# Kernel optimization log

Measured on AMD Instinct MI355X. Metric: run time of the kernel, lower is better.

The kernel has to match this reference:

```python
import jax, jax.numpy as jnp
import numpy as np

DIM = 128
N_CODES = 1024
N_STAGES = 4
BATCH, SEQ = 16, 8192


def setup_inputs() -> dict:
    key = jax.random.key(0)
    k1, k2 = jax.random.split(key)
    x_real = jax.random.normal(k1, (BATCH, SEQ, DIM), dtype=jnp.float32)
    codebooks = jax.random.normal(k2, (N_STAGES, N_CODES, DIM), dtype=jnp.float32) * 0.02
    return {"x_real": x_real, "codebooks": codebooks}


def reference(x_real, codebooks):
    """Residual VQ: per stage compute L2 dists via matmul+norms, argmin, gather.
    Returns (quantized [B,S,dim], indices [n_stages,B,S] int32)."""
    Bshape = x_real.shape
    x_flat = x_real.reshape(-1, Bshape[-1])  # [N, dim]
    residual = x_flat
    quantized = jnp.zeros_like(x_flat)
    all_indices = []
    n_stages = codebooks.shape[0]
    for s in range(n_stages):  # small fixed stage count
        codes = codebooks[s]  # [n_codes, dim]
        dots = residual @ codes.T  # [N, n_codes]
        codes_norm = jnp.sum(codes ** 2, axis=1)[None, :]
        residual_norm = jnp.sum(residual ** 2, axis=1, keepdims=True)
        dists = residual_norm + codes_norm - 2.0 * dots
        indices = jnp.argmin(dists, axis=1)  # [N]
        chosen = codes[indices]  # [N, dim] gather
        quantized = quantized + chosen
        residual = residual - chosen
        all_indices.append(indices.reshape(Bshape[:-1]))
    q = quantized.reshape(Bshape)
    return q, jnp.stack(all_indices, axis=0)
```

## Files before the change

### kernel.cpp

```cpp
#include <hip/hip_runtime.h>
#include <hip/hip_bf16.h>
#include <math.h>

constexpr int DIM = 128;
constexpr int NC = 1024;
constexpr int NS = 4;
constexpr int NVEC = 16 * 8192;
constexpr size_t QSIZE = (size_t)NVEC * DIM;
constexpr int BM = 64;
constexpr int CAP = 32;
constexpr float MARGIN = 0.125f;
constexpr int RS = DIM + 1;
constexpr int GSZ = 8 * 64 * 8;

typedef short bf16x8 __attribute__((ext_vector_type(8)));
typedef float f32x16 __attribute__((ext_vector_type(16)));

__device__ __forceinline__ short f2bf(float f) {
    __hip_bfloat16 h = __float2bfloat16(f);
    union { __hip_bfloat16 h; short s; } u;
    u.h = h;
    return u.s;
}

__device__ __forceinline__ short f2bf_fast(float f) {
    unsigned u = __float_as_uint(f);
    unsigned r = (u + 0x7FFFu + ((u >> 16) & 1u)) >> 16;
    return (short)r;
}

__device__ __forceinline__ unsigned fmap(float f) {
    unsigned u = __float_as_uint(f);
    return (u & 0x80000000u) ? ~u : (u | 0x80000000u);
}
__device__ __forceinline__ float funmap(unsigned k) {
    unsigned u = (k & 0x80000000u) ? (k & 0x7FFFFFFFu) : ~k;
    return __uint_as_float(u);
}

template <typename PTR>
__device__ __forceinline__ float np_pairwise_sq128(PTR v) {
#pragma clang fp contract(off)
    float r[8];
#pragma unroll
    for (int j = 0; j < 8; ++j) { float sq = v[j] * v[j]; r[j] = sq; }
#pragma unroll
    for (int i = 8; i < DIM; i += 8) {
#pragma unroll
        for (int j = 0; j < 8; ++j) { float sq = v[i + j] * v[i + j]; r[j] = r[j] + sq; }
    }
    return ((r[0] + r[1]) + (r[2] + r[3])) + ((r[4] + r[5]) + (r[6] + r[7]));
}

__device__ __forceinline__ float exact_dist(const float* __restrict__ rv,
                                            const float* __restrict__ cp,
                                            float rn, float cn) {
    float a0 = 0.f;
#pragma unroll
    for (int d = 0; d < DIM; d += 4) {
        float4 q = *(const float4*)(cp + d);
        a0 = __builtin_fmaf(rv[d], q.x, a0);
        a0 = __builtin_fmaf(rv[d + 1], q.y, a0);
        a0 = __builtin_fmaf(rv[d + 2], q.z, a0);
        a0 = __builtin_fmaf(rv[d + 3], q.w, a0);
    }
    return (rn + cn) - 2.0f * a0;
}

__global__ __launch_bounds__(256) void rvq_norms(
        const float* __restrict__ cb, float* __restrict__ cnorm) {
    int row = blockIdx.x * 256 + threadIdx.x;
    if (row >= NS * NC) return;
    cnorm[row] = np_pairwise_sq128(cb + (size_t)row * DIM);
}

__global__ __launch_bounds__(256) void rvq_swizzle(
        const float* __restrict__ cb, short* __restrict__ swz) {
    int bg = blockIdx.x;
    const float* src = cb + (size_t)bg * 32 * DIM;
    short* dst = swz + (size_t)bg * GSZ;
    int t = threadIdx.x;
#pragma unroll
    for (int i = 0; i < 2; ++i) {
        int o = t * 16 + i * 8;
        int ks = o >> 9;
        int l = (o >> 3) & 63;
        const float* p = src + (l & 31) * DIM + ks * 16 + (l >> 5) * 8;
        bf16x8 v;
#pragma unroll
        for (int j = 0; j < 8; ++j) v[j] = f2bf(p[j]);
        *(bf16x8*)(dst + o) = v;
    }
}

__global__ __launch_bounds__(256, 3) void rvq_main(
        const float* __restrict__ x,
        const float* __restrict__ cb,
        const short* __restrict__ swz,
        const float* __restrict__ cnorm_ws,
        float* __restrict__ out) {
    __shared__ float s_res[BM * RS];
    __shared__ float s_cnorm[NC];
    __shared__ unsigned s_vmin[BM];
    __shared__ unsigned short s_cand[BM * CAP];
    __shared__ unsigned long long s_best[BM];
    __shared__ float s_rn[BM];
    __shared__ int s_cnt[BM];
    __shared__ int s_ovf[BM];
    __shared__ int s_idx[BM];
    __shared__ int s_ovlist[BM];
    __shared__ int s_ovn;

    const int tid = threadIdx.x;
    const int w = tid >> 6;
    const int l = tid & 63;
    const int l31 = l & 31;
    const int h = l >> 5;
    const int Q = w * 256;
    const int blockbase = blockIdx.x * BM;

    for (int i4 = tid; i4 < BM * DIM / 4; i4 += 256) {
        int vec = i4 >> 5, d4 = (i4 & 31) * 4;
        float4 t = *(const float4*)(x + (size_t)(blockbase + vec) * DIM + d4);
        float* rp = &s_res[vec * RS + d4];
        rp[0] = t.x; rp[1] = t.y; rp[2] = t.z; rp[3] = t.w;
    }

#pragma unroll 1
    for (int s = 0; s < NS; ++s) {
        for (int i = tid; i < NC; i += 256) s_cnorm[i] = cnorm_ws[s * NC + i];
        if (tid < BM) {
            s_cnt[tid] = 0; s_ovf[tid] = 0; s_vmin[tid] = 0xFFFFFFFFu;
            s_best[tid] = ~0ull;
        }
        if (tid == 0) s_ovn = 0;
        __syncthreads();

        if (tid < BM) s_rn[tid] = np_pairwise_sq128(&s_res[tid * RS]);

        bf16x8 breg[2][8];
#pragma unroll
        for (int tc = 0; tc < 2; ++tc) {
            const float* p = &s_res[(tc * 32 + l31) * RS + h * 8];
#pragma unroll
            for (int ks = 0; ks < 8; ++ks) {
                bf16x8 b;
#pragma unroll
                for (int j = 0; j < 8; ++j) b[j] = f2bf_fast(p[ks * 16 + j]);
                breg[tc][ks] = b;
            }
        }

        const short* swz_s = swz + (size_t)s * 32 * GSZ;
        float vthr[2];
        float runmin[2] = { INFINITY, INFINITY };

#pragma unroll 1
        for (int pass = 0; pass < 2; ++pass) {
#pragma unroll 2
            for (int sub = 0; sub < 8; ++sub) {
                const int cbase = Q + sub * 32;
                const short* ap = swz_s + (size_t)(w * 8 + sub) * GSZ;
                f32x16 acc0, acc1;
#pragma unroll
                for (int j = 0; j < 16; ++j) { acc0[j] = 0.f; acc1[j] = 0.f; }
#pragma unroll
                for (int ks = 0; ks < 8; ++ks) {
                    bf16x8 a = *(const bf16x8*)(ap + ks * 512 + l * 8);
                    acc0 = __builtin_amdgcn_mfma_f32_32x32x16_bf16(a, breg[0][ks], acc0, 0, 0, 0);
                    acc1 = __builtin_amdgcn_mfma_f32_32x32x16_bf16(a, breg[1][ks], acc1, 0, 0, 0);
                }
                float4 cnq[4];
#pragma unroll
                for (int q = 0; q < 4; ++q)
                    cnq[q] = *(const float4*)&s_cnorm[cbase + 4 * h + 8 * q];
                if (pass == 0) {
#pragma unroll
                    for (int r = 0; r < 16; ++r) {
                        float sc0 = fmaf(acc0[r], -2.f, cnq[r >> 2][r & 3]);
                        float sc1 = fmaf(acc1[r], -2.f, cnq[r >> 2][r & 3]);
                        runmin[0] = fminf(runmin[0], sc0);
                        runmin[1] = fminf(runmin[1], sc1);
                    }
                } else {
#pragma unroll
                    for (int r = 0; r < 16; ++r) {
                        float sc0 = fmaf(acc0[r], -2.f, cnq[r >> 2][r & 3]);
                        float sc1 = fmaf(acc1[r], -2.f, cnq[r >> 2][r & 3]);
                        int code = cbase + (r & 3) + 8 * (r >> 2) + 4 * h;
                        if (sc0 <= vthr[0]) {
                            int o = atomicAdd(&s_cnt[l31], 1);
                            if (o < CAP) s_cand[l31 * CAP + o] = (unsigned short)code;
                            else s_ovf[l31] = 1;
                        }
                        if (sc1 <= vthr[1]) {
                            int o = atomicAdd(&s_cnt[32 + l31], 1);
                            if (o < CAP) s_cand[(32 + l31) * CAP + o] = (unsigned short)code;
                            else s_ovf[32 + l31] = 1;
                        }
                    }
                }
            }
            if (pass == 0) {
                atomicMin(&s_vmin[l31], fmap(runmin[0]));
                atomicMin(&s_vmin[32 + l31], fmap(runmin[1]));
                __syncthreads();
                vthr[0] = funmap(s_vmin[l31]) + MARGIN;
                vthr[1] = funmap(s_vmin[32 + l31]) + MARGIN;
            }
        }
        __syncthreads();

        {
            int vec = l;
            int n = s_cnt[vec];
            if (!s_ovf[vec]) {
                if (n == 1) {
                    if (w == 0) s_idx[vec] = s_cand[vec * CAP];
                } else {
                    const float* rv = &s_res[vec * RS];
                    float rn = s_rn[vec];
                    for (int k = w; k < n; k += 4) {
                        int c = s_cand[vec * CAP + k];
                        float dist = exact_dist(rv, cb + ((size_t)s * NC + c) * DIM,
                                                rn, s_cnorm[c]);
                        unsigned long long pack =
                            ((unsigned long long)fmap(dist) << 32) | (unsigned)c;
                        atomicMin(&s_best[vec], pack);
                    }
                }
            }
        }
        __syncthreads();
        if (tid < BM && !s_ovf[tid] && s_cnt[tid] > 1)
            s_idx[tid] = (int)(unsigned)(s_best[tid] & 0xFFFFFFFFull);
        if (tid < BM && s_ovf[tid]) {
            int p = atomicAdd(&s_ovn, 1);
            s_ovlist[p] = tid;
        }
        __syncthreads();
        for (int o = w; o < s_ovn; o += 4) {
            int vec = s_ovlist[o];
            const float* rv = &s_res[vec * RS];
            float rn = s_rn[vec];
            float best = INFINITY; int bidx = 0;
            for (int k = 0; k < 16; ++k) {
                int c = k * 64 + l;
                float dist = exact_dist(rv, cb + ((size_t)s * NC + c) * DIM,
                                        rn, s_cnorm[c]);
                if (dist < best) { best = dist; bidx = c; }
            }
#pragma unroll
            for (int off = 32; off >= 1; off >>= 1) {
                float ob = __shfl_xor(best, off, 64);
                int oi = __shfl_xor(bidx, off, 64);
                if (ob < best || (ob == best && oi < bidx)) { best = ob; bidx = oi; }
            }
            if (l == 0) s_idx[vec] = bidx;
        }
        __syncthreads();

        if (s < NS - 1) {
            for (int i4 = tid; i4 < BM * DIM / 4; i4 += 256) {
                int vec = i4 >> 5, d4 = (i4 & 31) * 4;
                int c = s_idx[vec];
                float4 cc = *(const float4*)(cb + ((size_t)s * NC + c) * DIM + d4);
                float* rp = &s_res[vec * RS + d4];
                rp[0] = rp[0] - cc.x; rp[1] = rp[1] - cc.y;
                rp[2] = rp[2] - cc.z; rp[3] = rp[3] - cc.w;
            }
        } else {
            for (int i4 = tid; i4 < BM * DIM / 4; i4 += 256) {
                int vec = i4 >> 5, d4 = (i4 & 31) * 4;
                int c = s_idx[vec];
                float4 cc = *(const float4*)(cb + ((size_t)s * NC + c) * DIM + d4);
                float4 xx = *(const float4*)(x + (size_t)(blockbase + vec) * DIM + d4);
                const float* rp = &s_res[vec * RS + d4];
                float4 oo;
                oo.x = xx.x - (rp[0] - cc.x); oo.y = xx.y - (rp[1] - cc.y);
                oo.z = xx.z - (rp[2] - cc.z); oo.w = xx.w - (rp[3] - cc.w);
                *(float4*)(out + (size_t)(blockbase + vec) * DIM + d4) = oo;
            }
        }
        if (tid < BM)
            out[QSIZE + (size_t)s * NVEC + blockbase + tid] = (float)s_idx[tid];
        __syncthreads();
    }
}

extern "C" void kernel_launch(void* const* d_in, const int* in_sizes, int n_in,
                              void* d_out, int out_size, void* d_ws, size_t ws_size,
                              hipStream_t stream) {
    const float* x  = (const float*)d_in[0];
    const float* cb = (const float*)d_in[1];
    short* swz = (short*)d_ws;
    float* cnorm = (float*)((char*)d_ws + (size_t)NS * NC * DIM * sizeof(short));
    float* out = (float*)d_out;

    rvq_norms<<<(NS * NC + 255) / 256, 256, 0, stream>>>(cb, cnorm);
    rvq_swizzle<<<NS * 32, 256, 0, stream>>>(cb, swz);
    rvq_main<<<NVEC / BM, 256, 0, stream>>>(x, cb, swz, cnorm, out);
}
```

Before: 566.1 us.

## Replace two-pass threshold search with single-pass running-min candidate filtering

The nearest-code search now runs the MFMA distance tiles once per stage instead of twice. Each lane combines its tile minimum with a shared running minimum (via atomicMin) to get a threshold, and candidates are stored with their scores. A serial pass then prunes them against the final threshold before exact re-ranking. The block tile drops from 64 to 32 vectors and the launch bound rises to 5 waves per EU to improve occupancy. The risk is that early, looser thresholds admit more candidates, so the CAP=32 list can overflow more often and trigger the slower exact fallback.

```diff
diff --git a/kernel.cpp b/kernel.cpp
--- a/kernel.cpp
+++ b/kernel.cpp
@@ -7,7 +7,7 @@
 constexpr int NS = 4;
 constexpr int NVEC = 16 * 8192;
 constexpr size_t QSIZE = (size_t)NVEC * DIM;
-constexpr int BM = 64;
+constexpr int BM = 32;
 constexpr int CAP = 32;
 constexpr float MARGIN = 0.125f;
 constexpr int RS = DIM + 1;
@@ -93,7 +93,7 @@
     }
 }
 
-__global__ __launch_bounds__(256, 3) void rvq_main(
+__global__ __launch_bounds__(256, 5) void rvq_main(
         const float* __restrict__ x,
         const float* __restrict__ cb,
         const short* __restrict__ swz,
@@ -102,7 +102,7 @@
     __shared__ float s_res[BM * RS];
     __shared__ float s_cnorm[NC];
     __shared__ unsigned s_vmin[BM];
-    __shared__ unsigned short s_cand[BM * CAP];
+    __shared__ unsigned long long s_cand[BM * CAP];
     __shared__ unsigned long long s_best[BM];
     __shared__ float s_rn[BM];
     __shared__ int s_cnt[BM];
@@ -138,95 +138,92 @@
 
         if (tid < BM) s_rn[tid] = np_pairwise_sq128(&s_res[tid * RS]);
 
-        bf16x8 breg[2][8];
-#pragma unroll
-        for (int tc = 0; tc < 2; ++tc) {
-            const float* p = &s_res[(tc * 32 + l31) * RS + h * 8];
+        bf16x8 breg[8];
+        {
+            const float* p = &s_res[l31 * RS + h * 8];
 #pragma unroll
             for (int ks = 0; ks < 8; ++ks) {
                 bf16x8 b;
 #pragma unroll
                 for (int j = 0; j < 8; ++j) b[j] = f2bf_fast(p[ks * 16 + j]);
-                breg[tc][ks] = b;
+                breg[ks] = b;
             }
         }
 
         const short* swz_s = swz + (size_t)s * 32 * GSZ;
-        float vthr[2];
-        float runmin[2] = { INFINITY, INFINITY };
-
-#pragma unroll 1
-        for (int pass = 0; pass < 2; ++pass) {
+
 #pragma unroll 2
-            for (int sub = 0; sub < 8; ++sub) {
-                const int cbase = Q + sub * 32;
-                const short* ap = swz_s + (size_t)(w * 8 + sub) * GSZ;
-                f32x16 acc0, acc1;
-#pragma unroll
-                for (int j = 0; j < 16; ++j) { acc0[j] = 0.f; acc1[j] = 0.f; }
-#pragma unroll
-                for (int ks = 0; ks < 8; ++ks) {
-                    bf16x8 a = *(const bf16x8*)(ap + ks * 512 + l * 8);
-                    acc0 = __builtin_amdgcn_mfma_f32_32x32x16_bf16(a, breg[0][ks], acc0, 0, 0, 0);
-                    acc1 = __builtin_amdgcn_mfma_f32_32x32x16_bf16(a, breg[1][ks], acc1, 0, 0, 0);
+        for (int sub = 0; sub < 8; ++sub) {
+            const int cbase = Q + sub * 32;
+            const short* ap = swz_s + (size_t)(w * 8 + sub) * GSZ;
+            f32x16 acc;
+#pragma unroll
+            for (int j = 0; j < 16; ++j) acc[j] = 0.f;
+#pragma unroll
+            for (int ks = 0; ks < 8; ++ks) {
+                bf16x8 a = *(const bf16x8*)(ap + ks * 512 + l * 8);
+                acc = __builtin_amdgcn_mfma_f32_32x32x16_bf16(a, breg[ks], acc, 0, 0, 0);
+            }
+            float4 cnq[4];
+#pragma unroll
+            for (int q = 0; q < 4; ++q)
+                cnq[q] = *(const float4*)&s_cnorm[cbase + 4 * h + 8 * q];
+            float sc[16];
+#pragma unroll
+            for (int r = 0; r < 16; ++r)
+                sc[r] = fmaf(acc[r], -2.f, cnq[r >> 2][r & 3]);
+            float m0 = fminf(fminf(sc[0], sc[1]), fminf(sc[2], sc[3]));
+            float m1 = fminf(fminf(sc[4], sc[5]), fminf(sc[6], sc[7]));
+            float m2 = fminf(fminf(sc[8], sc[9]), fminf(sc[10], sc[11]));
+            float m3 = fminf(fminf(sc[12], sc[13]), fminf(sc[14], sc[15]));
+            float lmin = fminf(fminf(m0, m1), fminf(m2, m3));
+            unsigned mymap = fmap(lmin);
+            unsigned cur = atomicMin(&s_vmin[l31], mymap);
+            unsigned tU = cur < mymap ? cur : mymap;
+            float thr = funmap(tU) + MARGIN;
+#pragma unroll
+            for (int r = 0; r < 16; ++r) {
+                if (sc[r] <= thr) {
+                    int code = cbase + (r & 3) + 8 * (r >> 2) + 4 * h;
+                    int o = atomicAdd(&s_cnt[l31], 1);
+                    if (o < CAP)
+                        s_cand[l31 * CAP + o] =
+                            ((unsigned long long)fmap(sc[r]) << 32) | (unsigned)code;
+                    else s_ovf[l31] = 1;
                 }
-                float4 cnq[4];
-#pragma unroll
-                for (int q = 0; q < 4; ++q)
-                    cnq[q] = *(const float4*)&s_cnorm[cbase + 4 * h + 8 * q];
-                if (pass == 0) {
-#pragma unroll
-                    for (int r = 0; r < 16; ++r) {
-                        float sc0 = fmaf(acc0[r], -2.f, cnq[r >> 2][r & 3]);
-                        float sc1 = fmaf(acc1[r], -2.f, cnq[r >> 2][r & 3]);
-                        runmin[0] = fminf(runmin[0], sc0);
-                        runmin[1] = fminf(runmin[1], sc1);
-                    }
-                } else {
-#pragma unroll
-                    for (int r = 0; r < 16; ++r) {
-                        float sc0 = fmaf(acc0[r], -2.f, cnq[r >> 2][r & 3]);
-                        float sc1 = fmaf(acc1[r], -2.f, cnq[r >> 2][r & 3]);
-                        int code = cbase + (r & 3) + 8 * (r >> 2) + 4 * h;
-                        if (sc0 <= vthr[0]) {
-                            int o = atomicAdd(&s_cnt[l31], 1);
-                            if (o < CAP) s_cand[l31 * CAP + o] = (unsigned short)code;
-                            else s_ovf[l31] = 1;
-                        }
-                        if (sc1 <= vthr[1]) {
-                            int o = atomicAdd(&s_cnt[32 + l31], 1);
-                            if (o < CAP) s_cand[(32 + l31) * CAP + o] = (unsigned short)code;
-                            else s_ovf[32 + l31] = 1;
-                        }
-                    }
+            }
+        }
+        __syncthreads();
+
+        if (tid < BM && !s_ovf[tid]) {
+            int n = s_cnt[tid];
+            unsigned thrF = fmap(funmap(s_vmin[tid]) + MARGIN);
+            int m = 0;
+            unsigned long long keep = 0;
+            for (int j = 0; j < n; ++j) {
+                unsigned long long pk = s_cand[tid * CAP + j];
+                if ((unsigned)(pk >> 32) <= thrF) {
+                    s_cand[tid * CAP + m] = pk; keep = pk; ++m;
                 }
             }
-            if (pass == 0) {
-                atomicMin(&s_vmin[l31], fmap(runmin[0]));
-                atomicMin(&s_vmin[32 + l31], fmap(runmin[1]));
-                __syncthreads();
-                vthr[0] = funmap(s_vmin[l31]) + MARGIN;
-                vthr[1] = funmap(s_vmin[32 + l31]) + MARGIN;
-            }
+            s_cnt[tid] = m;
+            if (m == 1) s_idx[tid] = (int)(unsigned)(keep & 0xFFFFFFFFull);
         }
         __syncthreads();
 
         {
-            int vec = l;
-            int n = s_cnt[vec];
+            int vec = l31;
             if (!s_ovf[vec]) {
-                if (n == 1) {
-                    if (w == 0) s_idx[vec] = s_cand[vec * CAP];
-                } else {
+                int m = s_cnt[vec];
+                if (m >= 2) {
                     const float* rv = &s_res[vec * RS];
                     float rn = s_rn[vec];
-                    for (int k = w; k < n; k += 4) {
-                        int c = s_cand[vec * CAP + k];
+                    for (int k = w * 2 + h; k < m; k += 8) {
+                        int c = (int)(unsigned)(s_cand[vec * CAP + k] & 0xFFFFFFFFull);
                         float dist = exact_dist(rv, cb + ((size_t)s * NC + c) * DIM,
                                                 rn, s_cnorm[c]);
-                        unsigned long long pack =
-                            ((unsigned long long)fmap(dist) << 32) | (unsigned)c;
-                        atomicMin(&s_best[vec], pack);
+                        atomicMin(&s_best[vec],
+                                  ((unsigned long long)fmap(dist) << 32) | (unsigned)c);
                     }
                 }
             }
```

Result: slower. 1.007 ms (+77.9%).

## Replace two-pass MFMA distance scan with single pass using running atomic min threshold

Applied to the files above, without the earlier changes.

Drops the first pass that computed each vector's min approximate distance over all codes before a second MFMA pass collected candidates. Now each 32-code subtile computes its local min, folds it into a shared atomicMin, and uses the current running min plus margin as the candidate threshold, so the MFMA work is done once. The cost is that early subtiles see a looser threshold, which admits more candidates, raises the chance of CAP overflow, and makes the exact-distance fallback run more often. The occupancy hint of 3 waves in launch_bounds is also removed.

```diff
diff --git a/kernel.cpp b/kernel.cpp
--- a/kernel.cpp
+++ b/kernel.cpp
@@ -93,7 +93,7 @@
     }
 }
 
-__global__ __launch_bounds__(256, 3) void rvq_main(
+__global__ __launch_bounds__(256) void rvq_main(
         const float* __restrict__ x,
         const float* __restrict__ cb,
         const short* __restrict__ swz,
@@ -152,81 +152,66 @@
         }
 
         const short* swz_s = swz + (size_t)s * 32 * GSZ;
-        float vthr[2];
-        float runmin[2] = { INFINITY, INFINITY };
-
-#pragma unroll 1
-        for (int pass = 0; pass < 2; ++pass) {
+
 #pragma unroll 2
-            for (int sub = 0; sub < 8; ++sub) {
-                const int cbase = Q + sub * 32;
-                const short* ap = swz_s + (size_t)(w * 8 + sub) * GSZ;
-                f32x16 acc0, acc1;
-#pragma unroll
-                for (int j = 0; j < 16; ++j) { acc0[j] = 0.f; acc1[j] = 0.f; }
-#pragma unroll
-                for (int ks = 0; ks < 8; ++ks) {
-                    bf16x8 a = *(const bf16x8*)(ap + ks * 512 + l * 8);
-                    acc0 = __builtin_amdgcn_mfma_f32_32x32x16_bf16(a, breg[0][ks], acc0, 0, 0, 0);
-                    acc1 = __builtin_amdgcn_mfma_f32_32x32x16_bf16(a, breg[1][ks], acc1, 0, 0, 0);
+        for (int sub = 0; sub < 8; ++sub) {
+            const int cbase = Q + sub * 32;
+            const short* ap = swz_s + (size_t)(w * 8 + sub) * GSZ;
+            f32x16 acc0, acc1;
+#pragma unroll
+            for (int j = 0; j < 16; ++j) { acc0[j] = 0.f; acc1[j] = 0.f; }
+#pragma unroll
+            for (int ks = 0; ks < 8; ++ks) {
+                bf16x8 a = *(const bf16x8*)(ap + ks * 512 + l * 8);
+                acc0 = __builtin_amdgcn_mfma_f32_32x32x16_bf16(a, breg[0][ks], acc0, 0, 0, 0);
+                acc1 = __builtin_amdgcn_mfma_f32_32x32x16_bf16(a, breg[1][ks], acc1, 0, 0, 0);
+            }
+            float lm0 = INFINITY, lm1 = INFINITY;
+#pragma unroll
+            for (int r = 0; r < 16; ++r) {
+                int code = cbase + (r & 3) + 8 * (r >> 2) + 4 * h;
+                lm0 = fminf(lm0, fmaf(acc0[r], -2.f, s_cnorm[code]));
+                lm1 = fminf(lm1, fmaf(acc1[r], -2.f, s_cnorm[code]));
+            }
+            unsigned my0 = fmap(lm0), my1 = fmap(lm1);
+            unsigned c0 = atomicMin(&s_vmin[l31], my0);
+            unsigned c1 = atomicMin(&s_vmin[32 + l31], my1);
+            float thr0 = funmap(c0 < my0 ? c0 : my0) + MARGIN;
+            float thr1 = funmap(c1 < my1 ? c1 : my1) + MARGIN;
+#pragma unroll
+            for (int r = 0; r < 16; ++r) {
+                int code = cbase + (r & 3) + 8 * (r >> 2) + 4 * h;
+                float sc0 = fmaf(acc0[r], -2.f, s_cnorm[code]);
+                float sc1 = fmaf(acc1[r], -2.f, s_cnorm[code]);
+                if (sc0 <= thr0) {
+                    int o = atomicAdd(&s_cnt[l31], 1);
+                    if (o < CAP) s_cand[l31 * CAP + o] = (unsigned short)code;
+                    else s_ovf[l31] = 1;
                 }
-                float4 cnq[4];
-#pragma unroll
-                for (int q = 0; q < 4; ++q)
-                    cnq[q] = *(const float4*)&s_cnorm[cbase + 4 * h + 8 * q];
-                if (pass == 0) {
-#pragma unroll
-                    for (int r = 0; r < 16; ++r) {
-                        float sc0 = fmaf(acc0[r], -2.f, cnq[r >> 2][r & 3]);
-                        float sc1 = fmaf(acc1[r], -2.f, cnq[r >> 2][r & 3]);
-                        runmin[0] = fminf(runmin[0], sc0);
-                        runmin[1] = fminf(runmin[1], sc1);
-                    }
-                } else {
-#pragma unroll
-                    for (int r = 0; r < 16; ++r) {
-                        float sc0 = fmaf(acc0[r], -2.f, cnq[r >> 2][r & 3]);
-                        float sc1 = fmaf(acc1[r], -2.f, cnq[r >> 2][r & 3]);
-                        int code = cbase + (r & 3) + 8 * (r >> 2) + 4 * h;
-                        if (sc0 <= vthr[0]) {
-                            int o = atomicAdd(&s_cnt[l31], 1);
-                            if (o < CAP) s_cand[l31 * CAP + o] = (unsigned short)code;
-                            else s_ovf[l31] = 1;
-                        }
-                        if (sc1 <= vthr[1]) {
-                            int o = atomicAdd(&s_cnt[32 + l31], 1);
-                            if (o < CAP) s_cand[(32 + l31) * CAP + o] = (unsigned short)code;
-                            else s_ovf[32 + l31] = 1;
-                        }
-                    }
+                if (sc1 <= thr1) {
+                    int o = atomicAdd(&s_cnt[32 + l31], 1);
+                    if (o < CAP) s_cand[(32 + l31) * CAP + o] = (unsigned short)code;
+                    else s_ovf[32 + l31] = 1;
                 }
             }
-            if (pass == 0) {
-                atomicMin(&s_vmin[l31], fmap(runmin[0]));
-                atomicMin(&s_vmin[32 + l31], fmap(runmin[1]));
-                __syncthreads();
-                vthr[0] = funmap(s_vmin[l31]) + MARGIN;
-                vthr[1] = funmap(s_vmin[32 + l31]) + MARGIN;
-            }
-        }
-        __syncthreads();
-
+        }
+        __syncthreads();
+
+        if (tid < BM && !s_ovf[tid] && s_cnt[tid] == 1)
+            s_idx[tid] = s_cand[tid * CAP];
         {
             int vec = l;
-            int n = s_cnt[vec];
             if (!s_ovf[vec]) {
-                if (n == 1) {
-                    if (w == 0) s_idx[vec] = s_cand[vec * CAP];
-                } else {
+                int m = s_cnt[vec];
+                if (m >= 2) {
                     const float* rv = &s_res[vec * RS];
                     float rn = s_rn[vec];
-                    for (int k = w; k < n; k += 4) {
+                    for (int k = w; k < m; k += 4) {
                         int c = s_cand[vec * CAP + k];
                         float dist = exact_dist(rv, cb + ((size_t)s * NC + c) * DIM,
                                                 rn, s_cnorm[c]);
-                        unsigned long long pack =
-                            ((unsigned long long)fmap(dist) << 32) | (unsigned)c;
-                        atomicMin(&s_best[vec], pack);
+                        atomicMin(&s_best[vec],
+                                  ((unsigned long long)fmap(dist) << 32) | (unsigned)c);
                     }
                 }
             }
```

Result: slower. 1.135 ms (+100.5%).
